# Kernel optimization log

Hardware: AMD Instinct MI355X
Metric: run time of the kernel (lower is better)

Reference implementation:

```python
import jax, jax.numpy as jnp
import numpy as np
import math

B, T, D, H = 2, 4096, 1024, 16
DH = D // H
LOCAL = 3
MAX_GATE = 0.6


def dilated_positions(seq_len, local=LOCAL):
    A = local + int(math.ceil(math.log2(max(seq_len, 2)))) + 1
    pos = np.zeros((seq_len, A), np.int32)
    msk = np.zeros((seq_len, A), bool)
    for i in range(seq_len):
        ap = [i] + [i - j for j in range(1, local + 1) if i - j >= 0]
        k = 2
        while 2 ** k <= i:
            ap.append(i - 2 ** k)
            k += 1
        pos[i, :len(ap)] = ap
        msk[i, :len(ap)] = True
    return pos, msk


def pid_proj(x, Wp, Wi, Wd, Wg, bg):
    # x: (B,T,D); W*: (D,D); Wg: (D,3); bg: (3,)
    t = x.shape[1]
    denom = jnp.arange(1, t + 1, dtype=x.dtype)[None, :, None]
    integral = jnp.cumsum(x, axis=1) / denom
    derivative = jnp.concatenate([jnp.zeros_like(x[:, :1]), x[:, 1:] - x[:, :-1]], axis=1)
    g = jax.nn.softmax(x @ Wg + bg, axis=-1)
    g = jnp.minimum(g, MAX_GATE)
    g = g / g.sum(axis=-1, keepdims=True)
    return g[..., 0:1] * (x @ Wp) + g[..., 1:2] * (integral @ Wi) + g[..., 2:3] * (derivative @ Wd)


def setup_inputs() -> dict:
    key = jax.random.key(0)
    ks = jax.random.split(key, 16)
    s = 1.0 / math.sqrt(D)
    inp = {"x": jax.random.normal(ks[0], (B, T, D), jnp.float32)}
    i = 1
    for name in ("q", "k", "v"):
        inp[f"Wp_{name}"] = jax.random.normal(ks[i], (D, D), jnp.float32) * s; i += 1
        inp[f"Wi_{name}"] = jax.random.normal(ks[i], (D, D), jnp.float32) * s * 0.3; i += 1
        inp[f"Wd_{name}"] = jax.random.normal(ks[i], (D, D), jnp.float32) * s * 0.3; i += 1
        inp[f"Wg_{name}"] = jax.random.normal(ks[i], (D, 3), jnp.float32) * s; i += 1
        inp[f"bg_{name}"] = jnp.array([0.5, 0.0, 0.0], jnp.float32)
    inp["Wo"] = jax.random.normal(ks[13], (D, D), jnp.float32) * s
    pos, msk = dilated_positions(T)
    inp["positions"] = jnp.asarray(pos)
    inp["mask"] = jnp.asarray(msk)
    return inp


def reference(x, Wp_q, Wi_q, Wd_q, Wg_q, bg_q,
              Wp_k, Wi_k, Wd_k, Wg_k, bg_k,
              Wp_v, Wi_v, Wd_v, Wg_v, bg_v,
              Wo, positions, mask):
    b, t, d = x.shape
    scale = DH ** -0.5
    def heads(y):  # (B,T,D) -> (B,H,T,DH)
        return y.reshape(b, t, H, DH).transpose(0, 2, 1, 3)
    q = heads(pid_proj(x, Wp_q, Wi_q, Wd_q, Wg_q, bg_q))
    k = heads(pid_proj(x, Wp_k, Wi_k, Wd_k, Wg_k, bg_k))
    v = heads(pid_proj(x, Wp_v, Wi_v, Wd_v, Wg_v, bg_v))
    # gather per-query sparse K/V: (B,H,T,A,DH)
    k_sparse = k[:, :, positions]
    v_sparse = v[:, :, positions]
    scores = jnp.einsum('bhsd,bhsad->bhsa', q, k_sparse) * scale
    scores = jnp.where(mask[None, None], scores, -jnp.inf)
    attn = jax.nn.softmax(scores, axis=-1)
    out = jnp.einsum('bhsa,bhsad->bhsd', attn, v_sparse)
    out = out.transpose(0, 2, 1, 3).reshape(b, t, d)
    return out @ Wo
```

## Files before the change

### kernel.cpp

```cpp
#include <hip/hip_runtime.h>
#include <hip/hip_bf16.h>
#include <cstdint>

#define B_   2
#define T_   4096
#define D_   1024
#define H_   16
#define DH_  64
#define M_   (B_*T_)
#define K3_  (3*D_)
#define TC_  128
#define NCH_ (T_/TC_)

typedef __attribute__((ext_vector_type(4))) float  f32x4;
typedef __attribute__((ext_vector_type(8))) short  short8;

__device__ __forceinline__ float bf2f(ushort u) {
    union { uint32_t i; float f; } v; v.i = ((uint32_t)u) << 16; return v.f;
}
__device__ __forceinline__ ushort f2bf(float f) {
    union { float f; uint32_t i; } v; v.f = f;
    uint32_t r = v.i + 0x7FFF + ((v.i >> 16) & 1);
    return (ushort)(r >> 16);
}

template<bool F32>
__device__ __forceinline__ float ld_in(const void* p, size_t i) {
    if (F32) return ((const float*)p)[i];
    return bf2f(((const ushort*)p)[i]);
}

__device__ __forceinline__ void st_c(ushort* p, float v) { *p = f2bf(v); }
__device__ __forceinline__ void st_c(float*  p, float v) { *p = v; }

#define GLOAD_LDS16(g, l) \
    __builtin_amdgcn_global_load_lds((const __attribute__((address_space(1))) void*)(g), \
                                     (__attribute__((address_space(3))) void*)(l), 16, 0, 0)

__global__ void detect_kernel(const ushort* __restrict__ xu, int* __restrict__ flag) {
    __shared__ int cnt;
    if (threadIdx.x == 0) cnt = 0;
    __syncthreads();
    int c = 0;
    for (int i = threadIdx.x; i < 16384; i += 256) {
        ushort u = xu[i];
        if ((u & 0x7F80) == 0x7F80) c++;
    }
    if (c) atomicAdd(&cnt, c);
    __syncthreads();
    if (threadIdx.x == 0) flag[0] = (cnt > 0) ? 1 : 0;
}

template<bool F32>
__device__ __forceinline__ void gates_body(const void* x,
                                           const void* Wg_q, const void* bg_q,
                                           const void* Wg_k, const void* bg_k,
                                           const void* Wg_v, const void* bg_v,
                                           float* __restrict__ g9) {
    const int wave = threadIdx.x >> 6, lane = threadIdx.x & 63;
    const int row  = blockIdx.x * 4 + wave;
    const size_t xoff = (size_t)row * D_;
    float acc[9] = {0,0,0,0,0,0,0,0,0};
    for (int d = lane; d < D_; d += 64) {
        float xv = ld_in<F32>(x, xoff + d);
        #pragma unroll
        for (int c = 0; c < 3; c++) {
            acc[0+c] += xv * ld_in<F32>(Wg_q, d*3+c);
            acc[3+c] += xv * ld_in<F32>(Wg_k, d*3+c);
            acc[6+c] += xv * ld_in<F32>(Wg_v, d*3+c);
        }
    }
    #pragma unroll
    for (int i = 0; i < 9; i++) {
        #pragma unroll
        for (int o = 32; o >= 1; o >>= 1) acc[i] += __shfl_xor(acc[i], o, 64);
    }
    const void* bgs[3] = {bg_q, bg_k, bg_v};
    float g[9];
    #pragma unroll
    for (int p = 0; p < 3; p++) {
        float l0 = acc[p*3+0] + ld_in<F32>(bgs[p], 0);
        float l1 = acc[p*3+1] + ld_in<F32>(bgs[p], 1);
        float l2 = acc[p*3+2] + ld_in<F32>(bgs[p], 2);
        float mx = fmaxf(l0, fmaxf(l1, l2));
        float e0 = expf(l0-mx), e1 = expf(l1-mx), e2 = expf(l2-mx);
        float s  = e0+e1+e2;
        float g0 = fminf(e0/s, 0.6f), g1 = fminf(e1/s, 0.6f), g2 = fminf(e2/s, 0.6f);
        float s2 = g0+g1+g2;
        g0 /= s2; g1 /= s2; g2 /= s2;
        float g1c = fmaxf(g1, 1e-30f), g2c = fmaxf(g2, 1e-30f);
        g[p*3+0] = g0 / g1c;
        g[p*3+1] = g1c / g2c;
        g[p*3+2] = g2c;
    }
    if (lane == 0) {
        #pragma unroll
        for (int i = 0; i < 9; i++) g9[(size_t)row*9 + i] = g[i];
    }
}
__global__ void gates_kernel(const void* x,
                             const void* Wg_q, const void* bg_q,
                             const void* Wg_k, const void* bg_k,
                             const void* Wg_v, const void* bg_v,
                             const int* __restrict__ flag, float* __restrict__ g9) {
    if (flag[0]) gates_body<true >(x, Wg_q, bg_q, Wg_k, bg_k, Wg_v, bg_v, g9);
    else         gates_body<false>(x, Wg_q, bg_q, Wg_k, bg_k, Wg_v, bg_v, g9);
}

template<bool F32>
__device__ __forceinline__ void chunk_sum_body(const void* x, float* __restrict__ part) {
    const int d = blockIdx.x * 256 + threadIdx.x;
    const int tc = blockIdx.y, b = blockIdx.z;
    const size_t base = ((size_t)b*T_ + (size_t)tc*TC_) * D_ + d;
    float s = 0.f;
    for (int i = 0; i < TC_; i++) s += ld_in<F32>(x, base + (size_t)i * D_);
    part[((size_t)b*NCH_ + tc) * D_ + d] = s;
}
__global__ void chunk_sum_kernel(const void* x, const int* __restrict__ flag,
                                 float* __restrict__ part) {
    if (flag[0]) chunk_sum_body<true >(x, part);
    else         chunk_sum_body<false>(x, part);
}

__global__ void scan_part_kernel(float* __restrict__ part) {
    const int idx = blockIdx.x * 256 + threadIdx.x;
    const int b = idx >> 10, d = idx & (D_-1);
    float run = 0.f;
    for (int tc = 0; tc < NCH_; tc++) {
        size_t o = ((size_t)b*NCH_ + tc) * D_ + d;
        float v = part[o]; part[o] = run; run += v;
    }
}

template<bool F32>
__device__ __forceinline__ void build_xs_body(const void* x, const float* __restrict__ part,
                                              ushort* __restrict__ Xc) {
    const int d0 = (blockIdx.x * 256 + threadIdx.x) * 2;
    const int tc = blockIdx.y, b = blockIdx.z;
    const int t0 = tc * TC_;
    float carry0 = part[((size_t)b*NCH_ + tc) * D_ + d0];
    float carry1 = part[((size_t)b*NCH_ + tc) * D_ + d0 + 1];
    const size_t xbase = ((size_t)b*T_ + t0) * D_ + d0;
    float prev0 = (t0 > 0) ? ld_in<F32>(x, xbase - D_)     : 0.0f;
    float prev1 = (t0 > 0) ? ld_in<F32>(x, xbase - D_ + 1) : 0.0f;
    for (int i = 0; i < TC_; i++) {
        const int t = t0 + i;
        float xv0 = ld_in<F32>(x, xbase + (size_t)i * D_);
        float xv1 = ld_in<F32>(x, xbase + (size_t)i * D_ + 1);
        carry0 += xv0; carry1 += xv1;
        const float rinv = 1.0f / (float)(t + 1);
        float in0 = carry0 * rinv, in1 = carry1 * rinv;
        float de0 = (t == 0) ? 0.0f : (xv0 - prev0);
        float de1 = (t == 0) ? 0.0f : (xv1 - prev1);
        prev0 = xv0; prev1 = xv1;
        const size_t base = ((size_t)b*T_ + t) * K3_ + d0;
        *(ushort2*)(Xc + base       ) = make_ushort2(f2bf(xv0), f2bf(xv1));
        *(ushort2*)(Xc + base +   D_) = make_ushort2(f2bf(in0), f2bf(in1));
        *(ushort2*)(Xc + base + 2*D_) = make_ushort2(f2bf(de0), f2bf(de1));
    }
}
__global__ void build_xs_kernel(const void* x, const float* __restrict__ part,
                                const int* __restrict__ flag, ushort* __restrict__ Xc) {
    if (flag[0]) build_xs_body<true >(x, part, Xc);
    else         build_xs_body<false>(x, part, Xc);
}

struct WPtrs { const void* w[10]; };
template<bool F32>
__device__ __forceinline__ void transpose_w_body(WPtrs ptrs, ushort* __restrict__ Wt,
                                                 ushort* __restrict__ WoT) {
    const int z = blockIdx.z;
    const void* src = ptrs.w[z];
    __shared__ float tile[32][33];
    const int tx = threadIdx.x & 31, ty = threadIdx.x >> 5;
    const int d0 = blockIdx.x * 32, c0 = blockIdx.y * 32;
    #pragma unroll
    for (int i = 0; i < 4; i++) {
        int r = ty + i*8;
        tile[r][tx] = ld_in<F32>(src, (size_t)(d0 + r) * D_ + c0 + tx);
    }
    __syncthreads();
    if (z < 9) {
        const int p = z / 3, j = z % 3;
        #pragma unroll
        for (int i = 0; i < 4; i++) {
            int r = ty + i*8;
            Wt[(size_t)(p*D_ + c0 + r) * K3_ + j*D_ + d0 + tx] = f2bf(tile[tx][r]);
        }
    } else {
        #pragma unroll
        for (int i = 0; i < 4; i++) {
            int r = ty + i*8;
            WoT[(size_t)(c0 + r) * D_ + d0 + tx] = f2bf(tile[tx][r]);
        }
    }
}
__global__ void transpose_w_kernel(WPtrs ptrs, const int* __restrict__ flag,
                                   ushort* __restrict__ Wt, ushort* __restrict__ WoT) {
    if (flag[0]) transpose_w_body<true >(ptrs, Wt, WoT);
    else         transpose_w_body<false>(ptrs, Wt, WoT);
}

__global__ __launch_bounds__(512, 2) void gemm_qkv_kernel(
        const ushort* __restrict__ Abase,
        const ushort* __restrict__ Bt,
        ushort* __restrict__ C,
        const float* __restrict__ g9) {
    constexpr int SUBE = 16384;
    constexpr int NS   = K3_ / 32;
    constexpr int RSTR = 128 * K3_;
    __shared__ __align__(16) ushort LDS[4 * SUBE];
    const int tid  = threadIdx.x;
    const int lane = tid & 63;
    const int wave = tid >> 6;
    const int wm   = wave >> 2;
    const int wn   = wave & 3;
    const int quad = lane >> 4, l16 = lane & 15;
    const int gq   = quad ^ ((l16 >> 1) & 3);

    const int wg = (blockIdx.x % 8) * 48 + blockIdx.x / 8;
    const int mt = wg & 31;
    const int nt = wg >> 5;
    const int m0 = mt * 256;
    const int n0 = nt * 256;
    const int p  = n0 >> 10;

    const int arow = tid >> 2;
    const int acg  = (tid & 3) ^ ((arow >> 1) & 3);
    const ushort* pA = Abase + (size_t)(m0 + arow) * K3_ + acg * 8;
    const ushort* pB = Bt    + (size_t)(n0 + arow) * K3_ + acg * 8;
    const int l8 = tid * 8;

    int ard[8], brd[4];
    #pragma unroll
    for (int i = 0; i < 8; i++) ard[i] = (wm*128 + i*16 + l16) * 32 + gq*8;
    #pragma unroll
    for (int j = 0; j < 4; j++) brd[j] = 8192 + (wn*64 + j*16 + l16) * 32 + gq*8;

    f32x4 acc[8][4] = {};

    #pragma unroll
    for (int s = 0; s < 3; s++) {
        const int base = s * SUBE;
        GLOAD_LDS16(pA + s*32,        &LDS[base + l8]);
        GLOAD_LDS16(pA + RSTR + s*32, &LDS[base + l8 + 4096]);
        GLOAD_LDS16(pB + s*32,        &LDS[base + 8192 + l8]);
        GLOAD_LDS16(pB + RSTR + s*32, &LDS[base + 8192 + l8 + 4096]);
    }
    asm volatile("s_waitcnt vmcnt(8)" ::: "memory");
    __builtin_amdgcn_s_barrier();

    for (int s = 0; s < NS; ++s) {
        const int bs = (s & 3) * SUBE;
        const int sb = ((s + 3) & 3) * SUBE;
        const int sk = (s + 3) * 32;
        const bool stage = (s + 3 < NS);

        short8 af[4], bfr[4], af2[4];

        #pragma unroll
        for (int i = 0; i < 4; i++) af[i]  = *(const short8*)&LDS[bs + ard[i]];
        #pragma unroll
        for (int j = 0; j < 4; j++) bfr[j] = *(const short8*)&LDS[bs + brd[j]];
        if (stage) {
            GLOAD_LDS16(pA + sk,        &LDS[sb + l8]);
            GLOAD_LDS16(pA + RSTR + sk, &LDS[sb + l8 + 4096]);
        }
        asm volatile("s_waitcnt lgkmcnt(0)" ::: "memory");
        __builtin_amdgcn_sched_barrier(0);
        __builtin_amdgcn_s_setprio(1);
        #pragma unroll
        for (int i = 0; i < 4; i++)
            #pragma unroll
            for (int j = 0; j < 4; j++)
                acc[i][j] = __builtin_amdgcn_mfma_f32_16x16x32_bf16(af[i], bfr[j], acc[i][j], 0, 0, 0);
        __builtin_amdgcn_s_setprio(0);

        #pragma unroll
        for (int i = 0; i < 4; i++) af2[i] = *(const short8*)&LDS[bs + ard[i+4]];
        if (stage) {
            GLOAD_LDS16(pB + sk,        &LDS[sb + 8192 + l8]);
            GLOAD_LDS16(pB + RSTR + sk, &LDS[sb + 8192 + l8 + 4096]);
        }
        asm volatile("s_waitcnt lgkmcnt(0)" ::: "memory");
        __builtin_amdgcn_sched_barrier(0);
        __builtin_amdgcn_s_setprio(1);
        #pragma unroll
        for (int i = 0; i < 4; i++)
            #pragma unroll
            for (int j = 0; j < 4; j++)
                acc[4+i][j] = __builtin_amdgcn_mfma_f32_16x16x32_bf16(af2[i], bfr[j], acc[4+i][j], 0, 0, 0);
        __builtin_amdgcn_s_setprio(0);

        if (stage)             asm volatile("s_waitcnt vmcnt(8)" ::: "memory");
        else if (s + 3 == NS)  asm volatile("s_waitcnt vmcnt(4)" ::: "memory");
        else if (s + 2 == NS)  asm volatile("s_waitcnt vmcnt(0)" ::: "memory");
        __builtin_amdgcn_s_barrier();

        if ((s & 31) == 31) {
            const int seg = s >> 5;
            #pragma unroll
            for (int i = 0; i < 8; i++) {
                #pragma unroll
                for (int rg = 0; rg < 4; rg++) {
                    const int rrow = m0 + wm*128 + i*16 + quad*4 + rg;
                    const float gv = g9[(size_t)rrow * 9 + p*3 + seg];
                    #pragma unroll
                    for (int j = 0; j < 4; j++)
                        acc[i][j][rg] *= gv;
                }
            }
        }
    }

    #pragma unroll
    for (int i = 0; i < 8; i++) {
        #pragma unroll
        for (int j = 0; j < 4; j++) {
            const int rrow = m0 + wm*128 + i*16 + quad*4;
            const int col  = n0 + wn*64 + j*16 + l16;
            #pragma unroll
            for (int rg = 0; rg < 4; rg++)
                C[(size_t)(rrow + rg) * K3_ + col] = f2bf(acc[i][j][rg]);
        }
    }
}

template<typename CT, int NTILES, bool GATED>
__global__ __launch_bounds__(512, 2) void gemm_bt8_kernel(
        const ushort* __restrict__ Abase,
        const ushort* __restrict__ Bt,
        CT* __restrict__ C,
        const float* __restrict__ g9,
        int K, int lda, int ldc) {
    __shared__ __align__(16) ushort LDS[3 * 24576];
    const int tid  = threadIdx.x;
    const int lane = tid & 63;
    const int wave = tid >> 6;
    const int wm   = wave >> 2;
    const int wn   = wave & 3;
    const int quad = lane >> 4, l16 = lane & 15, sw = l16 & 7;

    const int MT     = M_ / 128;
    const int cpx    = (MT * NTILES) / 8;
    const int wg     = (blockIdx.x % 8) * cpx + blockIdx.x / 8;
    const int mchunk = MT / 8;
    const int rem    = wg % (mchunk * NTILES);
    const int mt     = (wg / (mchunk * NTILES)) * mchunk + (rem % mchunk);
    const int nt     = rem / mchunk;
    const int m0 = mt * 128;
    const int n0 = nt * 256;
    const int p  = n0 >> 10;

    const ushort* asrc[2]; int aoff[2];
    #pragma unroll
    for (int g = 0; g < 2; g++) {
        const int I = g*512 + tid;
        const int row = I >> 3, c8 = (I & 7) ^ (row & 7);
        asrc[g] = Abase + (size_t)(m0 + row) * lda + c8*8;
        aoff[g] = I * 8;
    }
    const ushort* bsrc[4]; int boff[4];
    #pragma unroll
    for (int g = 0; g < 4; g++) {
        const int I = g*512 + tid;
        const int row = I >> 3, c8 = (I & 7) ^ (row & 7);
        bsrc[g] = Bt + (size_t)(n0 + row) * K + c8*8;
        boff[g] = I * 8;
    }
    int ard[4], brd[4];
    #pragma unroll
    for (int i = 0; i < 4; i++) {
        ard[i] = (wm*64 + i*16 + l16) * 64;
        brd[i] = (wn*64 + i*16 + l16) * 64;
    }

    const int NKT = K >> 6;
    f32x4 acc[4][4] = {};

    #pragma unroll
    for (int g = 0; g < 2; g++) GLOAD_LDS16(asrc[g], &LDS[aoff[g]]);
    #pragma unroll
    for (int g = 0; g < 4; g++) GLOAD_LDS16(bsrc[g], &LDS[8192 + boff[g]]);
    #pragma unroll
    for (int g = 0; g < 2; g++) GLOAD_LDS16(asrc[g] + 64, &LDS[24576 + aoff[g]]);
    #pragma unroll
    for (int g = 0; g < 4; g++) GLOAD_LDS16(bsrc[g] + 64, &LDS[24576 + 8192 + boff[g]]);
    asm volatile("s_waitcnt vmcnt(6)" ::: "memory");
    __builtin_amdgcn_s_barrier();

    for (int t = 0; t < NKT; ++t) {
        const int cur = t % 3;
        const int ab  = cur * 24576;
        const int bb  = ab + 8192;
        const bool do_stage = (t + 2 < NKT);
        const int sb  = ((t + 2) % 3) * 24576;
        const int skt = (t + 2) << 6;

        short8 af[4], bfr[4];

        #pragma unroll
        for (int i = 0; i < 4; i++)
            af[i]  = *(const short8*)&LDS[ab + ard[i] + (quad ^ sw) * 8];
        #pragma unroll
        for (int j = 0; j < 4; j++)
            bfr[j] = *(const short8*)&LDS[bb + brd[j] + (quad ^ sw) * 8];
        if (do_stage) {
            GLOAD_LDS16(asrc[0] + skt, &LDS[sb + aoff[0]]);
            GLOAD_LDS16(asrc[1] + skt, &LDS[sb + aoff[1]]);
            GLOAD_LDS16(bsrc[0] + skt, &LDS[sb + 8192 + boff[0]]);
        }
        __builtin_amdgcn_s_barrier();
        asm volatile("s_waitcnt lgkmcnt(0)" ::: "memory");
        __builtin_amdgcn_sched_barrier(0);
        __builtin_amdgcn_s_setprio(1);
        #pragma unroll
        for (int i = 0; i < 4; i++)
            #pragma unroll
            for (int j = 0; j < 4; j++)
                acc[i][j] = __builtin_amdgcn_mfma_f32_16x16x32_bf16(af[i], bfr[j], acc[i][j], 0, 0, 0);
        __builtin_amdgcn_s_setprio(0);
        __builtin_amdgcn_s_barrier();

        #pragma unroll
        for (int i = 0; i < 4; i++)
            af[i]  = *(const short8*)&LDS[ab + ard[i] + ((quad + 4) ^ sw) * 8];
        #pragma unroll
        for (int j = 0; j < 4; j++)
            bfr[j] = *(const short8*)&LDS[bb + brd[j] + ((quad + 4) ^ sw) * 8];
        if (do_stage) {
            GLOAD_LDS16(bsrc[1] + skt, &LDS[sb + 8192 + boff[1]]);
            GLOAD_LDS16(bsrc[2] + skt, &LDS[sb + 8192 + boff[2]]);
            GLOAD_LDS16(bsrc[3] + skt, &LDS[sb + 8192 + boff[3]]);
        }
        __builtin_amdgcn_s_barrier();
        asm volatile("s_waitcnt lgkmcnt(0)" ::: "memory");
        __builtin_amdgcn_sched_barrier(0);
        __builtin_amdgcn_s_setprio(1);
        #pragma unroll
        for (int i = 0; i < 4; i++)
            #pragma unroll
            for (int j = 0; j < 4; j++)
                acc[i][j] = __builtin_amdgcn_mfma_f32_16x16x32_bf16(af[i], bfr[j], acc[i][j], 0, 0, 0);
        __builtin_amdgcn_s_setprio(0);
        if (do_stage)          asm volatile("s_waitcnt vmcnt(6)" ::: "memory");
        else if (t + 1 < NKT)  asm volatile("s_waitcnt vmcnt(0)" ::: "memory");
        __builtin_amdgcn_s_barrier();

        if (GATED && ((t & 15) == 15)) {
            const int seg = t >> 4;
            #pragma unroll
            for (int i = 0; i < 4; i++) {
                float gv[4];
                #pragma unroll
                for (int rg = 0; rg < 4; rg++) {
                    const int rrow = m0 + wm*64 + i*16 + quad*4 + rg;
                    gv[rg] = g9[(size_t)rrow * 9 + p*3 + seg];
                }
                #pragma unroll
                for (int j = 0; j < 4; j++)
                    #pragma unroll
                    for (int rg = 0; rg < 4; rg++)
                        acc[i][j][rg] *= gv[rg];
            }
        }
    }

    #pragma unroll
    for (int i = 0; i < 4; i++) {
        #pragma unroll
        for (int j = 0; j < 4; j++) {
            const int rrow = m0 + wm*64 + i*16 + quad*4;
            const int col  = n0 + wn*64 + j*16 + l16;
            #pragma unroll
            for (int rg = 0; rg < 4; rg++)
                st_c(&C[(size_t)(rrow + rg) * ldc + col], acc[i][j][rg]);
        }
    }
}

__global__ __launch_bounds__(256) void attn_kernel(const ushort* __restrict__ QKV,
                                                   ushort* __restrict__ AO) {
    const int tid = threadIdx.x;
    const int bt  = blockIdx.x;
    const int t   = bt & (T_-1);
    const size_t qrow = (size_t)bt * K3_;
    const int e0 = tid * 4;

    const ushort4 q4 = *(const ushort4*)(QKV + qrow + e0);
    const float qf0 = bf2f(q4.x), qf1 = bf2f(q4.y), qf2 = bf2f(q4.z), qf3 = bf2f(q4.w);

    float sc[14];
    #pragma unroll
    for (int a = 0; a < 14; a++) {
        const int off = (a <= 3) ? a : (1 << (a - 2));
        float p = -1e30f;
        if (off <= t) {
            const ushort4 k4 = *(const ushort4*)(QKV + qrow - (size_t)off*K3_ + D_ + e0);
            float pp = qf0*bf2f(k4.x) + qf1*bf2f(k4.y) + qf2*bf2f(k4.z) + qf3*bf2f(k4.w);
            pp += __shfl_xor(pp, 1, 64);
            pp += __shfl_xor(pp, 2, 64);
            pp += __shfl_xor(pp, 4, 64);
            pp += __shfl_xor(pp, 8, 64);
            p = pp * 0.125f;
        }
        sc[a] = p;
    }
    float mx = -1e30f;
    #pragma unroll
    for (int a = 0; a < 14; a++) mx = fmaxf(mx, sc[a]);
    float ev[14], s = 0.0f;
    #pragma unroll
    for (int a = 0; a < 14; a++) { ev[a] = (sc[a] > -1e29f) ? expf(sc[a] - mx) : 0.0f; s += ev[a]; }
    const float rs = 1.0f / s;

    float a0 = 0.f, a1 = 0.f, a2 = 0.f, a3 = 0.f;
    #pragma unroll
    for (int a = 0; a < 14; a++) {
        const int off = (a <= 3) ? a : (1 << (a - 2));
        if (off <= t) {
            const ushort4 v4 = *(const ushort4*)(QKV + qrow - (size_t)off*K3_ + 2*D_ + e0);
            const float w = ev[a] * rs;
            a0 += w * bf2f(v4.x); a1 += w * bf2f(v4.y);
            a2 += w * bf2f(v4.z); a3 += w * bf2f(v4.w);
        }
    }
    ushort* dst = AO + (size_t)bt * D_ + e0;
    dst[0] = f2bf(a0); dst[1] = f2bf(a1); dst[2] = f2bf(a2); dst[3] = f2bf(a3);
}

extern "C" void kernel_launch(void* const* d_in, const int* in_sizes, int n_in,
                              void* d_out, int out_size, void* d_ws, size_t ws_size,
                              hipStream_t stream) {
    (void)in_sizes; (void)n_in; (void)out_size; (void)ws_size;
    const void* x    = d_in[0];
    const void* Wg_q = d_in[4];  const void* bg_q = d_in[5];
    const void* Wg_k = d_in[9];  const void* bg_k = d_in[10];
    const void* Wg_v = d_in[14]; const void* bg_v = d_in[15];

    char* ws = (char*)d_ws;
    int*    flag = (int*)ws;    ws += 16;
    float*  g9   = (float*)ws;  ws += (size_t)M_*9*4;
    float*  part = (float*)ws;  ws += (size_t)B_*NCH_*D_*4;
    ushort* Wt   = (ushort*)ws; ws += (size_t)K3_*K3_*2;
    ushort* WoT  = (ushort*)ws; ws += (size_t)D_*D_*2;
    ushort* Xc   = (ushort*)ws; ws += (size_t)M_*K3_*2;
    ushort* QKV  = (ushort*)ws; ws += (size_t)M_*K3_*2;
    ushort* AO   = (ushort*)ws; ws += (size_t)M_*D_*2;

    detect_kernel<<<1, 256, 0, stream>>>((const ushort*)x, flag);
    gates_kernel<<<M_/4, 256, 0, stream>>>(x, Wg_q, bg_q, Wg_k, bg_k, Wg_v, bg_v, flag, g9);
    chunk_sum_kernel<<<dim3(D_/256, NCH_, B_), 256, 0, stream>>>(x, flag, part);
    scan_part_kernel<<<(B_*D_)/256, 256, 0, stream>>>(part);
    WPtrs wp;
    wp.w[0] = d_in[1];  wp.w[1] = d_in[2];  wp.w[2] = d_in[3];
    wp.w[3] = d_in[6];  wp.w[4] = d_in[7];  wp.w[5] = d_in[8];
    wp.w[6] = d_in[11]; wp.w[7] = d_in[12]; wp.w[8] = d_in[13];
    wp.w[9] = d_in[16];
    transpose_w_kernel<<<dim3(32, 32, 10), 256, 0, stream>>>(wp, flag, Wt, WoT);
    build_xs_kernel<<<dim3(D_/512, NCH_, B_), 256, 0, stream>>>(x, part, flag, Xc);
    gemm_qkv_kernel<<<384, 512, 0, stream>>>(Xc, Wt, QKV, g9);
    attn_kernel<<<B_*T_, 256, 0, stream>>>(QKV, AO);
    gemm_bt8_kernel<float, 4, false><<<256, 512, 0, stream>>>(AO, WoT, (float*)d_out, nullptr, D_, D_, D_);
}
```

Baseline: 517.4 us.

## Restructure QKV GEMM pipeline to double-buffered 64-wide K tiles with ping-pong barriers

Replaces the 4-stage, 32-wide K ring buffer in the fused QKV GEMM with a 2-buffer scheme. Each buffer holds a 64-wide K tile split into two 32-wide halves, and more s_barriers are interleaved between LDS reads, global-to-LDS loads and MFMA blocks to get a ping-pong schedule across waves. The change also alters the workgroup-to-tile mapping (4 M-tiles grouped per N sweep) and the LDS swizzle pattern. Prefetch depth drops and barriers are added, which may expose memory latency in exchange for the hoped-for better MFMA/load interleaving and L2 reuse.

```diff
diff --git a/kernel.cpp b/kernel.cpp
--- a/kernel.cpp
+++ b/kernel.cpp
@@ -206,66 +206,66 @@
         const ushort* __restrict__ Bt,
         ushort* __restrict__ C,
         const float* __restrict__ g9) {
-    constexpr int SUBE = 16384;
-    constexpr int NS   = K3_ / 32;
+    constexpr int NT   = K3_ / 64;
     constexpr int RSTR = 128 * K3_;
-    __shared__ __align__(16) ushort LDS[4 * SUBE];
+    __shared__ __align__(16) ushort LDS[2 * 32768];
     const int tid  = threadIdx.x;
     const int lane = tid & 63;
     const int wave = tid >> 6;
     const int wm   = wave >> 2;
     const int wn   = wave & 3;
     const int quad = lane >> 4, l16 = lane & 15;
-    const int gq   = quad ^ ((l16 >> 1) & 3);
-
-    const int wg = (blockIdx.x % 8) * 48 + blockIdx.x / 8;
-    const int mt = wg & 31;
-    const int nt = wg >> 5;
-    const int m0 = mt * 256;
-    const int n0 = nt * 256;
-    const int p  = n0 >> 10;
-
-    const int arow = tid >> 2;
-    const int acg  = (tid & 3) ^ ((arow >> 1) & 3);
-    const ushort* pA = Abase + (size_t)(m0 + arow) * K3_ + acg * 8;
-    const ushort* pB = Bt    + (size_t)(n0 + arow) * K3_ + acg * 8;
-    const int l8 = tid * 8;
-
-    int ard[8], brd[4];
-    #pragma unroll
-    for (int i = 0; i < 8; i++) ard[i] = (wm*128 + i*16 + l16) * 32 + gq*8;
-    #pragma unroll
-    for (int j = 0; j < 4; j++) brd[j] = 8192 + (wn*64 + j*16 + l16) * 32 + gq*8;
+    const int apos = (quad ^ (l16 >> 2)) * 8;
+
+    const int wg  = ((int)blockIdx.x % 8) * 48 + (int)blockIdx.x / 8;
+    const int rem = wg % 48;
+    const int mt  = (wg / 48) * 4 + (rem & 3);
+    const int nt  = rem >> 2;
+    const int m0  = mt * 256;
+    const int n0  = nt * 256;
+    const int p   = n0 >> 10;
+
+    const int j8 = ((tid & 3) ^ ((tid >> 4) & 3)) * 8;
+    const ushort* pA = Abase + (size_t)(m0 + (tid >> 2)) * K3_ + j8;
+    const ushort* pB = Bt    + (size_t)(n0 + (tid >> 2)) * K3_ + j8;
+    const int d0 = tid * 8;
+    const int d1 = (512 + tid) * 8;
+
+    int arow[8], brow[4];
+    #pragma unroll
+    for (int i = 0; i < 8; i++) arow[i] = (wm*128 + i*16 + l16) * 32;
+    #pragma unroll
+    for (int j = 0; j < 4; j++) brow[j] = 16384 + (wn*64 + j*16 + l16) * 32;
 
     f32x4 acc[8][4] = {};
 
-    #pragma unroll
-    for (int s = 0; s < 3; s++) {
-        const int base = s * SUBE;
-        GLOAD_LDS16(pA + s*32,        &LDS[base + l8]);
-        GLOAD_LDS16(pA + RSTR + s*32, &LDS[base + l8 + 4096]);
-        GLOAD_LDS16(pB + s*32,        &LDS[base + 8192 + l8]);
-        GLOAD_LDS16(pB + RSTR + s*32, &LDS[base + 8192 + l8 + 4096]);
-    }
-    asm volatile("s_waitcnt vmcnt(8)" ::: "memory");
+    GLOAD_LDS16(pA,             &LDS[d0]);
+    GLOAD_LDS16(pA + RSTR,      &LDS[d1]);
+    GLOAD_LDS16(pB,             &LDS[16384 + d0]);
+    GLOAD_LDS16(pB + RSTR,      &LDS[16384 + d1]);
+    GLOAD_LDS16(pA + 32,        &LDS[8192 + d0]);
+    GLOAD_LDS16(pA + RSTR + 32, &LDS[8192 + d1]);
+    GLOAD_LDS16(pB + 32,        &LDS[24576 + d0]);
+    GLOAD_LDS16(pB + RSTR + 32, &LDS[24576 + d1]);
+    asm volatile("s_waitcnt vmcnt(4)" ::: "memory");
     __builtin_amdgcn_s_barrier();
 
-    for (int s = 0; s < NS; ++s) {
-        const int bs = (s & 3) * SUBE;
-        const int sb = ((s + 3) & 3) * SUBE;
-        const int sk = (s + 3) * 32;
-        const bool stage = (s + 3 < NS);
-
-        short8 af[4], bfr[4], af2[4];
-
-        #pragma unroll
-        for (int i = 0; i < 4; i++) af[i]  = *(const short8*)&LDS[bs + ard[i]];
-        #pragma unroll
-        for (int j = 0; j < 4; j++) bfr[j] = *(const short8*)&LDS[bs + brd[j]];
+    for (int t = 0; t < NT; ++t) {
+        const int bb = (t & 1) << 15;
+        const int sb = bb ^ 32768;
+        const int sk = (t + 1) * 64;
+        const bool stage = (t + 1 < NT);
+        short8 af[4], bfr[4];
+
+        #pragma unroll
+        for (int i = 0; i < 4; i++) af[i]  = *(const short8*)&LDS[bb + arow[i] + apos];
+        #pragma unroll
+        for (int j = 0; j < 4; j++) bfr[j] = *(const short8*)&LDS[bb + brow[j] + apos];
         if (stage) {
-            GLOAD_LDS16(pA + sk,        &LDS[sb + l8]);
-            GLOAD_LDS16(pA + RSTR + sk, &LDS[sb + l8 + 4096]);
-        }
+            GLOAD_LDS16(pA + sk,        &LDS[sb + d0]);
+            GLOAD_LDS16(pA + RSTR + sk, &LDS[sb + d1]);
+        }
+        __builtin_amdgcn_s_barrier();
         asm volatile("s_waitcnt lgkmcnt(0)" ::: "memory");
         __builtin_amdgcn_sched_barrier(0);
         __builtin_amdgcn_s_setprio(1);
@@ -275,13 +275,15 @@
             for (int j = 0; j < 4; j++)
                 acc[i][j] = __builtin_amdgcn_mfma_f32_16x16x32_bf16(af[i], bfr[j], acc[i][j], 0, 0, 0);
         __builtin_amdgcn_s_setprio(0);
-
-        #pragma unroll
-        for (int i = 0; i < 4; i++) af2[i] = *(const short8*)&LDS[bs + ard[i+4]];
+        __builtin_amdgcn_s_barrier();
+
+        #pragma unroll
+        for (int i = 0; i < 4; i++) af[i] = *(const short8*)&LDS[bb + arow[i+4] + apos];
         if (stage) {
-            GLOAD_LDS16(pB + sk,        &LDS[sb + 8192 + l8]);
-            GLOAD_LDS16(pB + RSTR + sk, &LDS[sb + 8192 + l8 + 4096]);
-        }
+            GLOAD_LDS16(pB + sk,        &LDS[sb + 16384 + d0]);
+            GLOAD_LDS16(pB + RSTR + sk, &LDS[sb + 16384 + d1]);
+        }
+        __builtin_amdgcn_s_barrier();
         asm volatile("s_waitcnt lgkmcnt(0)" ::: "memory");
         __builtin_amdgcn_sched_barrier(0);
         __builtin_amdgcn_s_setprio(1);
@@ -289,16 +291,53 @@
         for (int i = 0; i < 4; i++)
             #pragma unroll
             for (int j = 0; j < 4; j++)
-                acc[4+i][j] = __builtin_amdgcn_mfma_f32_16x16x32_bf16(af2[i], bfr[j], acc[4+i][j], 0, 0, 0);
+                acc[4+i][j] = __builtin_amdgcn_mfma_f32_16x16x32_bf16(af[i], bfr[j], acc[4+i][j], 0, 0, 0);
         __builtin_amdgcn_s_setprio(0);
-
-        if (stage)             asm volatile("s_waitcnt vmcnt(8)" ::: "memory");
-        else if (s + 3 == NS)  asm volatile("s_waitcnt vmcnt(4)" ::: "memory");
-        else if (s + 2 == NS)  asm volatile("s_waitcnt vmcnt(0)" ::: "memory");
-        __builtin_amdgcn_s_barrier();
-
-        if ((s & 31) == 31) {
-            const int seg = s >> 5;
+        if (stage) asm volatile("s_waitcnt vmcnt(4)" ::: "memory");
+        else       asm volatile("s_waitcnt vmcnt(0)" ::: "memory");
+        __builtin_amdgcn_s_barrier();
+
+        #pragma unroll
+        for (int i = 0; i < 4; i++) af[i]  = *(const short8*)&LDS[bb + 8192 + arow[i] + apos];
+        #pragma unroll
+        for (int j = 0; j < 4; j++) bfr[j] = *(const short8*)&LDS[bb + 8192 + brow[j] + apos];
+        if (stage) {
+            GLOAD_LDS16(pA + sk + 32,        &LDS[sb + 8192 + d0]);
+            GLOAD_LDS16(pA + RSTR + sk + 32, &LDS[sb + 8192 + d1]);
+        }
+        __builtin_amdgcn_s_barrier();
+        asm volatile("s_waitcnt lgkmcnt(0)" ::: "memory");
+        __builtin_amdgcn_sched_barrier(0);
+        __builtin_amdgcn_s_setprio(1);
+        #pragma unroll
+        for (int i = 0; i < 4; i++)
+            #pragma unroll
+            for (int j = 0; j < 4; j++)
+                acc[i][j] = __builtin_amdgcn_mfma_f32_16x16x32_bf16(af[i], bfr[j], acc[i][j], 0, 0, 0);
+        __builtin_amdgcn_s_setprio(0);
+        __builtin_amdgcn_s_barrier();
+
+        #pragma unroll
+        for (int i = 0; i < 4; i++) af[i] = *(const short8*)&LDS[bb + 8192 + arow[i+4] + apos];
+        if (stage) {
+            GLOAD_LDS16(pB + sk + 32,        &LDS[sb + 24576 + d0]);
+            GLOAD_LDS16(pB + RSTR + sk + 32, &LDS[sb + 24576 + d1]);
+        }
+        __builtin_amdgcn_s_barrier();
+        asm volatile("s_waitcnt lgkmcnt(0)" ::: "memory");
+        __builtin_amdgcn_sched_barrier(0);
+        __builtin_amdgcn_s_setprio(1);
+        #pragma unroll
+        for (int i = 0; i < 4; i++)
+            #pragma unroll
+            for (int j = 0; j < 4; j++)
+                acc[4+i][j] = __builtin_amdgcn_mfma_f32_16x16x32_bf16(af[i], bfr[j], acc[4+i][j], 0, 0, 0);
+        __builtin_amdgcn_s_setprio(0);
+        if (stage) asm volatile("s_waitcnt vmcnt(4)" ::: "memory");
+        __builtin_amdgcn_s_barrier();
+
+        if ((t & 15) == 15) {
+            const int seg = t >> 4;
             #pragma unroll
             for (int i = 0; i < 8; i++) {
                 #pragma unroll
```

Result: slower. 549.5 us (+6.2%).
